# Performance work log

Measured on AMD Instinct MI355X. Metric: run time of the kernel, lower is better.

Reference implementation:

```python
import jax, jax.numpy as jnp
import numpy as np

C = 0.1          # curvature
EPS = 1e-8
BN_EPS = 1e-5
MAX_NORM = 0.9

def batchnorm_train(x, gamma, beta):
    mu = jnp.mean(x, axis=0)
    var = jnp.var(x, axis=0)  # biased, matches torch BN normalization
    return gamma * (x - mu) * jax.lax.rsqrt(var + BN_EPS) + beta

def euclidean_to_poincare(x, c=C, max_norm=MAX_NORM):
    norm = jnp.linalg.norm(x, axis=-1, keepdims=True)
    zeros_mask = norm == 0
    safe_norm = jnp.where(zeros_mask, jnp.ones_like(norm), norm)
    sqrt_c = jnp.sqrt(jnp.asarray(c, x.dtype))
    scale = max_norm * jnp.tanh(sqrt_c * norm) / (sqrt_c * safe_norm)
    return jnp.where(zeros_mask, jnp.zeros_like(x), scale * x)

def poincare_to_euclidean(x, c=C):
    norms = jnp.linalg.norm(x, axis=-1, keepdims=True)
    norms = jnp.clip(norms, 1e-8, 1.0 - 1e-8)
    sqrt_c = jnp.sqrt(jnp.asarray(c, x.dtype))
    return x * jnp.arctanh(sqrt_c * norms) / (sqrt_c * norms)

def batch_poincare_exp_map(x, v, c=C):
    x_nsq = jnp.sum(x * x, axis=-1, keepdims=True)
    lambda_x = 2.0 / (1.0 - c * x_nsq + EPS)
    v_norm = jnp.linalg.norm(v, axis=-1, keepdims=True)
    v_norm = jnp.maximum(v_norm, EPS)
    sqrt_c = jnp.sqrt(jnp.asarray(c, x.dtype))
    scale = jnp.tanh(sqrt_c * lambda_x * v_norm / 2.0) / (sqrt_c * v_norm)
    sv = scale * v
    numerator = (1.0 - c * x_nsq) * sv
    x_sv = jnp.sum(x * sv, axis=-1, keepdims=True)
    sv_nsq = jnp.sum(sv * sv, axis=-1, keepdims=True)
    denom = 1.0 - 2.0 * c * x_sv + c * c * x_nsq * sv_nsq
    result = x + numerator / (denom + EPS)
    mask = jnp.all(jnp.isfinite(result), axis=-1, keepdims=True)
    return jnp.where(mask, result, jnp.zeros_like(result))

def batch_poincare_log_map(x, y, c=C):
    x_nsq = jnp.sum(x * x, axis=-1, keepdims=True)
    lambda_x = 2.0 / (1.0 - c * x_nsq + EPS)
    y_nsq = jnp.sum(y * y, axis=-1, keepdims=True)
    xy = jnp.sum(x * y, axis=-1, keepdims=True)
    numerator = (1.0 - 2.0 * c * xy + c * y_nsq) * x - (1.0 - c * x_nsq) * y
    denom = 1.0 - 2.0 * c * xy + c * c * x_nsq * y_nsq
    diff = numerator / (denom + EPS)
    diff_norm = jnp.linalg.norm(diff, axis=-1, keepdims=True)
    diff_norm = jnp.maximum(diff_norm, EPS)
    sqrt_c = jnp.sqrt(jnp.asarray(c, x.dtype))
    return 2.0 / (sqrt_c * lambda_x) * jnp.arctanh(sqrt_c * diff_norm) * diff / diff_norm

def setup_inputs() -> dict:
    key = jax.random.key(0)
    ks = jax.random.split(key, 8)
    B, D_IN, H, D_OUT = 8192, 1024, 2048, 1000
    x = jax.random.normal(ks[0], (B, D_IN), dtype=jnp.float32)
    # kaiming_normal fan_out: std = sqrt(2/fan_out) with fan_out = out_features
    W1 = jax.random.normal(ks[1], (H, D_IN), dtype=jnp.float32) * np.sqrt(2.0 / H)
    b1 = jnp.zeros((H,), jnp.float32)
    g1 = jnp.ones((H,), jnp.float32)
    be1 = jnp.zeros((H,), jnp.float32)
    W2 = jax.random.normal(ks[2], (H, H), dtype=jnp.float32) * np.sqrt(2.0 / H)
    b2 = jnp.zeros((H,), jnp.float32)
    g2 = jnp.ones((H,), jnp.float32)
    be2 = jnp.zeros((H,), jnp.float32)
    W3 = jax.random.normal(ks[3], (D_OUT, H), dtype=jnp.float32) * np.sqrt(2.0 / D_OUT)
    b3 = jnp.zeros((D_OUT,), jnp.float32)
    return {"x": x, "W1": W1, "b1": b1, "g1": g1, "be1": be1,
            "W2": W2, "b2": b2, "g2": g2, "be2": be2, "W3": W3, "b3": b3}

def reference(x, W1, b1, g1, be1, W2, b2, g2, be2, W3, b3):
    h1 = jax.nn.relu(batchnorm_train(x @ W1.T + b1, g1, be1))
    h1_hyp = euclidean_to_poincare(h1)
    origin = jnp.zeros_like(h1_hyp)
    h1_tan = batch_poincare_log_map(origin, h1_hyp)
    h2_tan = jax.nn.relu(batchnorm_train(h1_tan @ W2.T + b2, g2, be2))
    h2_hyp = batch_poincare_exp_map(origin, h2_tan)
    h2_euc = poincare_to_euclidean(h2_hyp)
    out = h2_euc @ W3.T + b3
    return jax.nn.log_softmax(out, axis=1)
```

## Files before the change

kernel.cpp:

```cpp
#include <hip/hip_runtime.h>

typedef __bf16 bf16x8 __attribute__((ext_vector_type(8)));
typedef float f32x16 __attribute__((ext_vector_type(16)));
typedef unsigned short us8 __attribute__((ext_vector_type(8)));

#define AS1 __attribute__((address_space(1)))
#define AS3 __attribute__((address_space(3)))

__device__ __forceinline__ unsigned short f2bf(float x) {
  unsigned int u = __float_as_uint(x);
  u += 0x7fffu + ((u >> 16) & 1u);
  return (unsigned short)(u >> 16);
}
__device__ __forceinline__ float bf2f(unsigned short u) {
  return __uint_as_float(((unsigned int)u) << 16);
}
__device__ __forceinline__ void async_copy16(const void* g, void* l) {
  __builtin_amdgcn_global_load_lds((AS1 void*)(g), (AS3 void*)(l), 16, 0, 0);
}

#define BARRIER() asm volatile("s_barrier" ::: "memory")
#define WAITV(n) asm volatile("s_waitcnt vmcnt(" #n ")" ::: "memory")

__global__ void __launch_bounds__(256) k_prep(const float* __restrict__ x,
                                              const float* __restrict__ W1,
                                              const float* __restrict__ W2,
                                              const float* __restrict__ W3,
                                              unsigned short* __restrict__ Xb,
                                              unsigned short* __restrict__ W1b,
                                              unsigned short* __restrict__ W2b,
                                              unsigned short* __restrict__ W3b,
                                              float* __restrict__ P) {
  const long n1 = 2097152, n2 = 524288, n3 = 1048576, n4 = 524288;
  long i = (long)blockIdx.x * 256 + threadIdx.x;
  const float* s = nullptr;
  unsigned short* d = nullptr;
  long j = i;
  if (i < n1)                { s = x;  d = Xb; }
  else if ((j -= n1) < n2)   { s = W1; d = W1b; }
  else if ((j -= n2) < n3)   { s = W2; d = W2b; }
  else if ((j -= n3) < n4) {
    ushort4 o;
    if ((j >> 9) < 1000) {
      float4 v = ((const float4*)W3)[j];
      o.x = f2bf(v.x); o.y = f2bf(v.y); o.z = f2bf(v.z); o.w = f2bf(v.w);
    } else { o.x = 0; o.y = 0; o.z = 0; o.w = 0; }
    ((ushort4*)W3b)[j] = o;
    return;
  } else {
    j -= n4;
    ((float4*)P)[j] = (float4){0.f, 0.f, 0.f, 0.f};
    return;
  }
  float4 v = ((const float4*)s)[j];
  ushort4 o;
  o.x = f2bf(v.x); o.y = f2bf(v.y); o.z = f2bf(v.z); o.w = f2bf(v.w);
  ((ushort4*)d)[j] = o;
}

template <bool OUTBF16, bool STATS>
__global__ void __launch_bounds__(256, 1) k_gemm(const unsigned short* __restrict__ A,
                                                 const unsigned short* __restrict__ B,
                                                 void* __restrict__ Cout,
                                                 void* __restrict__ Cout2, int K,
                                                 int lda, int ldb, int ldc,
                                                 float* __restrict__ P) {
  __shared__ __align__(16) unsigned short lA[2][256 * 64];
  __shared__ __align__(16) unsigned short lB[2][256 * 64];
  const int tid = threadIdx.x;
  const int wave = tid >> 6;
  const int lane = tid & 63;
  const int l31 = lane & 31;
  const int khi = lane >> 5;
  const int r7 = l31 & 7;
  const int wrh = wave >> 1;
  const int wcn = wave & 1;

  const int f = blockIdx.x + gridDim.x * blockIdx.y;
  const int xcd = f & 7;
  const int fi = f >> 3;
  const int nblk = fi % gridDim.x;
  const int mblk = fi / gridDim.x + (gridDim.y >> 3) * xcd;
  const long m0 = (long)mblk * 256;
  const long n0 = (long)nblk * 256;
  const long koff = (long)blockIdx.z * K;
  const int NT = K >> 6;

  const int rsub = lane >> 3;
  const int qg = ((lane & 7) ^ rsub) * 8;
  const long lda8 = (long)lda * 8;
  const long ldb8 = (long)ldb * 8;
  const unsigned short* gAw = A + (m0 + wave * 64 + rsub) * (long)lda + koff + qg;
  const unsigned short* gBw = B + (n0 + wave * 64 + rsub) * (long)ldb + koff + qg;
  const int dW = (wave * 64) * 64;

  f32x16 acc[4][4];
#pragma unroll
  for (int i = 0; i < 4; ++i)
#pragma unroll
    for (int j = 0; j < 4; ++j) acc[i][j] = (f32x16)(0.f);

  auto stage = [&](int buf, long kk) {
    unsigned short* dA = &lA[buf][0] + dW;
    unsigned short* dB = &lB[buf][0] + dW;
#pragma unroll
    for (int i = 0; i < 8; ++i)
      async_copy16(gAw + (long)i * lda8 + kk, dA + i * 8 * 64);
#pragma unroll
    for (int i = 0; i < 8; ++i)
      async_copy16(gBw + (long)i * ldb8 + kk, dB + i * 8 * 64);
  };

  stage(0, 0);
  for (int t = 0; t < NT; ++t) {
    const unsigned short* lAc = &lA[t & 1][0];
    const unsigned short* lBc = &lB[t & 1][0];
    WAITV(0);
    BARRIER();
    if (t + 1 < NT) stage((t + 1) & 1, (long)(t + 1) * 64);
#pragma unroll
    for (int ks = 0; ks < 4; ++ks) {
      const int off = ((ks * 2 + khi) ^ r7) * 8;
      bf16x8 af[4], bfr[4];
#pragma unroll
      for (int m = 0; m < 4; ++m)
        af[m] = *(const bf16x8*)&lAc[(wrh * 128 + m * 32 + l31) * 64 + off];
#pragma unroll
      for (int n = 0; n < 4; ++n)
        bfr[n] = *(const bf16x8*)&lBc[(wcn * 128 + n * 32 + l31) * 64 + off];
#pragma unroll
      for (int m = 0; m < 4; ++m)
#pragma unroll
        for (int n = 0; n < 4; ++n)
          acc[m][n] = __builtin_amdgcn_mfma_f32_32x32x16_bf16(af[m], bfr[n], acc[m][n], 0, 0, 0);
    }
  }

  const int rbase = 4 * khi;
  const long crow0 = m0 + wrh * 128;
  const long ccol0 = n0 + wcn * 128;
  if (OUTBF16) {
    unsigned short* C = (unsigned short*)(blockIdx.z ? Cout2 : Cout);
#pragma unroll
    for (int m = 0; m < 4; ++m)
#pragma unroll
      for (int n = 0; n < 4; ++n) {
        long col = ccol0 + n * 32 + l31;
#pragma unroll
        for (int reg = 0; reg < 16; ++reg) {
          long row = crow0 + m * 32 + (reg & 3) + 8 * (reg >> 2) + rbase;
          C[row * (long)ldc + col] = f2bf(acc[m][n][reg]);
        }
      }
  } else {
    float* C = (float*)(blockIdx.z ? Cout2 : Cout);
#pragma unroll
    for (int m = 0; m < 4; ++m)
#pragma unroll
      for (int n = 0; n < 4; ++n) {
        long col = ccol0 + n * 32 + l31;
#pragma unroll
        for (int reg = 0; reg < 16; ++reg) {
          long row = crow0 + m * 32 + (reg & 3) + 8 * (reg >> 2) + rbase;
          C[row * (long)ldc + col] = acc[m][n][reg];
        }
      }
  }

  if (STATS) {
    float* sred = (float*)&lA[0][0];
    __syncthreads();
    sred[tid] = 0.f;
    sred[256 + tid] = 0.f;
    __syncthreads();
#pragma unroll
    for (int n = 0; n < 4; ++n) {
      float s = 0.f, s2 = 0.f;
#pragma unroll
      for (int m = 0; m < 4; ++m)
#pragma unroll
        for (int reg = 0; reg < 16; ++reg) {
          float v = acc[m][n][reg];
          s += v;
          s2 = fmaf(v, v, s2);
        }
      int cl = wcn * 128 + n * 32 + l31;
      atomicAdd(&sred[cl], s);
      atomicAdd(&sred[256 + cl], s2);
    }
    __syncthreads();
    atomicAdd(&P[n0 + tid], sred[tid]);
    atomicAdd(&P[2048 + n0 + tid], sred[256 + tid]);
  }
}

template <bool STAGE2>
__global__ void __launch_bounds__(256) k_fuse(const unsigned short* __restrict__ Zb,
                                              const float* __restrict__ P,
                                              const float* __restrict__ g,
                                              const float* __restrict__ be,
                                              unsigned short* __restrict__ Ab) {
  const int t = threadIdx.x, wave = t >> 6, lane = t & 63;
  const long row = (long)blockIdx.x * 4 + wave;

  float sc[32], sh[32];
#pragma unroll
  for (int c = 0; c < 4; ++c) {
    int b4 = (lane + 64 * c) * 2;
    float4 s0 = ((const float4*)P)[b4],       s1 = ((const float4*)P)[b4 + 1];
    float4 q0 = ((const float4*)P)[512 + b4], q1 = ((const float4*)P)[512 + b4 + 1];
    float4 g0 = ((const float4*)g)[b4],       g1 = ((const float4*)g)[b4 + 1];
    float4 e0 = ((const float4*)be)[b4],      e1 = ((const float4*)be)[b4 + 1];
    float sm[8] = {s0.x, s0.y, s0.z, s0.w, s1.x, s1.y, s1.z, s1.w};
    float sq[8] = {q0.x, q0.y, q0.z, q0.w, q1.x, q1.y, q1.z, q1.w};
    float gg[8] = {g0.x, g0.y, g0.z, g0.w, g1.x, g1.y, g1.z, g1.w};
    float bb[8] = {e0.x, e0.y, e0.z, e0.w, e1.x, e1.y, e1.z, e1.w};
#pragma unroll
    for (int j = 0; j < 8; ++j) {
      float mean = sm[j] * (1.f / 8192.f);
      float var = sq[j] * (1.f / 8192.f) - mean * mean;
      float a = gg[j] * rsqrtf(var + 1e-5f);
      sc[c * 8 + j] = a;
      sh[c * 8 + j] = bb[j] - mean * a;
    }
  }

  const us8* zr = (const us8*)(Zb + row * 2048);
  float v[32];
  float ss = 0.f;
#pragma unroll
  for (int c = 0; c < 4; ++c) {
    us8 z8 = zr[lane + 64 * c];
#pragma unroll
    for (int j = 0; j < 8; ++j) {
      float xv = fmaxf(fmaf(bf2f(z8[j]), sc[c * 8 + j], sh[c * 8 + j]), 0.f);
      v[c * 8 + j] = xv;
      ss = fmaf(xv, xv, ss);
    }
  }
#pragma unroll
  for (int o = 32; o > 0; o >>= 1) ss += __shfl_xor(ss, o, 64);
  float n2 = ss;

  const float rsc = 0.31622776601683794f;
  float fac;
  if (STAGE2) {
    float nn = sqrtf(n2);
    float vn = fmaxf(nn, 1e-8f);
    float tt = rsc * vn;
    float scl = tanhf(tt) / tt;
    float hn = scl * nn;
    float cn = fminf(fmaxf(hn, 1e-8f), 1.0f);
    float z = rsc * cn;
    fac = scl * (atanhf(z) / z);
  } else {
    fac = 0.f;
    if (n2 > 0.f) {
      float n = sqrtf(n2);
      float th = tanhf(rsc * n);
      float s = 0.9f * th / (rsc * n);
      float dn = fmaxf(s * n, 1e-8f);
      float z = rsc * dn;
      fac = -(atanhf(z) / z) * s;
    }
  }
  us8* dr = (us8*)(Ab + row * 2048);
#pragma unroll
  for (int c = 0; c < 4; ++c) {
    us8 o8;
#pragma unroll
    for (int j = 0; j < 8; ++j) o8[j] = f2bf(v[c * 8 + j] * fac);
    dr[lane + 64 * c] = o8;
  }
}

__global__ void __launch_bounds__(256) k_lsm(const unsigned short* __restrict__ Za,
                                             const unsigned short* __restrict__ Zb2,
                                             const float* __restrict__ b3,
                                             float* __restrict__ out) {
  const int t = threadIdx.x, wave = t >> 6, lane = t & 63;
  const long row = (long)blockIdx.x * 4 + wave;
  const unsigned short* za = Za + row * 1024;
  const unsigned short* zb = Zb2 + row * 1024;
  float v[16];
  float mx = -3.4e38f;
#pragma unroll
  for (int c = 0; c < 16; ++c) {
    int col = lane + 64 * c;
    if (col < 1000) {
      v[c] = bf2f(za[col]) + bf2f(zb[col]) + b3[col];
      mx = fmaxf(mx, v[c]);
    } else v[c] = -3.4e38f;
  }
#pragma unroll
  for (int o = 32; o > 0; o >>= 1) mx = fmaxf(mx, __shfl_xor(mx, o, 64));

  float se = 0.f;
#pragma unroll
  for (int c = 0; c < 16; ++c) {
    int col = lane + 64 * c;
    if (col < 1000) se += expf(v[c] - mx);
  }
#pragma unroll
  for (int o = 32; o > 0; o >>= 1) se += __shfl_xor(se, o, 64);
  float ls = logf(se);

  float* orow = out + row * 1000;
#pragma unroll
  for (int c = 0; c < 16; ++c) {
    int col = lane + 64 * c;
    if (col < 1000) orow[col] = v[c] - mx - ls;
  }
}

extern "C" void kernel_launch(void* const* d_in, const int* in_sizes, int n_in,
                              void* d_out, int out_size, void* d_ws, size_t ws_size,
                              hipStream_t stream) {
  (void)in_sizes; (void)n_in; (void)out_size; (void)ws_size;
  const float* x   = (const float*)d_in[0];
  const float* W1  = (const float*)d_in[1];
  const float* g1  = (const float*)d_in[3];
  const float* be1 = (const float*)d_in[4];
  const float* W2  = (const float*)d_in[5];
  const float* g2  = (const float*)d_in[7];
  const float* be2 = (const float*)d_in[8];
  const float* W3  = (const float*)d_in[9];
  const float* b3  = (const float*)d_in[10];
  float* out = (float*)d_out;

  char* ws = (char*)d_ws;
  size_t off = 0;
  auto alloc = [&](size_t bytes) {
    void* p = ws + off;
    off += (bytes + 255) & ~(size_t)255;
    return p;
  };
  unsigned short* Xb  = (unsigned short*)alloc((size_t)8192 * 1024 * 2);
  unsigned short* W1b = (unsigned short*)alloc((size_t)2048 * 1024 * 2);
  unsigned short* W2b = (unsigned short*)alloc((size_t)2048 * 2048 * 2);
  unsigned short* W3b = (unsigned short*)alloc((size_t)1024 * 2048 * 2);
  unsigned short* Zb  = (unsigned short*)alloc((size_t)8192 * 2048 * 2);
  unsigned short* Ab  = (unsigned short*)alloc((size_t)8192 * 2048 * 2);
  unsigned short* Z3a = (unsigned short*)alloc((size_t)8192 * 1024 * 2);
  float* P            = (float*)alloc((size_t)2 * 4096 * 4);
  float* P2 = P + 4096;
  unsigned short* Z3b = Zb;

  k_prep<<<16392, 256, 0, stream>>>(x, W1, W2, W3, Xb, W1b, W2b, W3b, P);

  k_gemm<true, true><<<dim3(8, 32, 1), 256, 0, stream>>>(Xb, W1b, Zb, Zb, 1024, 1024, 1024, 2048, P);
  k_fuse<false><<<2048, 256, 0, stream>>>(Zb, P, g1, be1, Ab);

  k_gemm<true, true><<<dim3(8, 32, 1), 256, 0, stream>>>(Ab, W2b, Zb, Zb, 2048, 2048, 2048, 2048, P2);
  k_fuse<true><<<2048, 256, 0, stream>>>(Zb, P2, g2, be2, Ab);

  k_gemm<true, false><<<dim3(4, 32, 2), 256, 0, stream>>>(Ab, W3b, Z3a, Z3b, 1024, 2048, 2048, 1024, nullptr);
  k_lsm<<<2048, 256, 0, stream>>>(Z3a, Z3b, b3, out);
}
```

Before: 336.3 us.

## Use 8 waves per GEMM block with 128x64 per-wave tiles

The GEMM block grows from 256 to 512 threads. The 256x256 tile is split across 8 waves in a 2x4 layout, so each wave computes 128x64 with half the accumulators. Global-to-LDS staging is redistributed across the 8 waves, and the column-statistics reduction is adjusted to match. This lowers register pressure and adds latency hiding per CU, at the cost of more LDS reads of the A fragments per useful MFMA and a launch bound asking for 2 blocks per CU, which the 128KB of LDS per block may not allow.

```diff
diff --git a/kernel.cpp b/kernel.cpp
--- a/kernel.cpp
+++ b/kernel.cpp
@@ -59,7 +59,7 @@
 }
 
 template <bool OUTBF16, bool STATS>
-__global__ void __launch_bounds__(256, 1) k_gemm(const unsigned short* __restrict__ A,
+__global__ void __launch_bounds__(512, 2) k_gemm(const unsigned short* __restrict__ A,
                                                  const unsigned short* __restrict__ B,
                                                  void* __restrict__ Cout,
                                                  void* __restrict__ Cout2, int K,
@@ -73,8 +73,8 @@
   const int l31 = lane & 31;
   const int khi = lane >> 5;
   const int r7 = l31 & 7;
-  const int wrh = wave >> 1;
-  const int wcn = wave & 1;
+  const int wrh = wave >> 2;
+  const int wcn = wave & 3;
 
   const int f = blockIdx.x + gridDim.x * blockIdx.y;
   const int xcd = f & 7;
@@ -88,27 +88,37 @@
 
   const int rsub = lane >> 3;
   const int qg = ((lane & 7) ^ rsub) * 8;
-  const long lda8 = (long)lda * 8;
-  const long ldb8 = (long)ldb * 8;
-  const unsigned short* gAw = A + (m0 + wave * 64 + rsub) * (long)lda + koff + qg;
-  const unsigned short* gBw = B + (n0 + wave * 64 + rsub) * (long)ldb + koff + qg;
-  const int dW = (wave * 64) * 64;
-
-  f32x16 acc[4][4];
+  const unsigned short* gAq0 = A + (m0 +       8 * wave + rsub) * (long)lda + koff + qg;
+  const unsigned short* gAq1 = A + (m0 +  64 + 8 * wave + rsub) * (long)lda + koff + qg;
+  const unsigned short* gAq2 = A + (m0 + 128 + 8 * wave + rsub) * (long)lda + koff + qg;
+  const unsigned short* gAq3 = A + (m0 + 192 + 8 * wave + rsub) * (long)lda + koff + qg;
+  const unsigned short* gB0  = B + (n0 + 32 * wave + rsub) * (long)ldb + koff + qg;
+  const unsigned short* gB1  = gB0 +  8 * (long)ldb;
+  const unsigned short* gB2  = gB0 + 16 * (long)ldb;
+  const unsigned short* gB3  = gB0 + 24 * (long)ldb;
+  const int dAq0 = (      8 * wave) * 64;
+  const int dAq1 = ( 64 + 8 * wave) * 64;
+  const int dAq2 = (128 + 8 * wave) * 64;
+  const int dAq3 = (192 + 8 * wave) * 64;
+  const int dB0  = (32 * wave) * 64;
+
+  f32x16 acc[4][2];
 #pragma unroll
   for (int i = 0; i < 4; ++i)
 #pragma unroll
-    for (int j = 0; j < 4; ++j) acc[i][j] = (f32x16)(0.f);
+    for (int j = 0; j < 2; ++j) acc[i][j] = (f32x16)(0.f);
 
   auto stage = [&](int buf, long kk) {
-    unsigned short* dA = &lA[buf][0] + dW;
-    unsigned short* dB = &lB[buf][0] + dW;
-#pragma unroll
-    for (int i = 0; i < 8; ++i)
-      async_copy16(gAw + (long)i * lda8 + kk, dA + i * 8 * 64);
-#pragma unroll
-    for (int i = 0; i < 8; ++i)
-      async_copy16(gBw + (long)i * ldb8 + kk, dB + i * 8 * 64);
+    unsigned short* lAn = &lA[buf][0];
+    unsigned short* lBn = &lB[buf][0];
+    async_copy16(gAq0 + kk, lAn + dAq0);
+    async_copy16(gAq1 + kk, lAn + dAq1);
+    async_copy16(gAq2 + kk, lAn + dAq2);
+    async_copy16(gAq3 + kk, lAn + dAq3);
+    async_copy16(gB0 + kk,  lBn + dB0);
+    async_copy16(gB1 + kk,  lBn + dB0 + 8 * 64);
+    async_copy16(gB2 + kk,  lBn + dB0 + 16 * 64);
+    async_copy16(gB3 + kk,  lBn + dB0 + 24 * 64);
   };
 
   stage(0, 0);
@@ -121,30 +131,30 @@
 #pragma unroll
     for (int ks = 0; ks < 4; ++ks) {
       const int off = ((ks * 2 + khi) ^ r7) * 8;
-      bf16x8 af[4], bfr[4];
+      bf16x8 af[4], bfr[2];
 #pragma unroll
       for (int m = 0; m < 4; ++m)
         af[m] = *(const bf16x8*)&lAc[(wrh * 128 + m * 32 + l31) * 64 + off];
 #pragma unroll
-      for (int n = 0; n < 4; ++n)
-        bfr[n] = *(const bf16x8*)&lBc[(wcn * 128 + n * 32 + l31) * 64 + off];
+      for (int n = 0; n < 2; ++n)
+        bfr[n] = *(const bf16x8*)&lBc[(wcn * 64 + n * 32 + l31) * 64 + off];
 #pragma unroll
       for (int m = 0; m < 4; ++m)
 #pragma unroll
-        for (int n = 0; n < 4; ++n)
+        for (int n = 0; n < 2; ++n)
           acc[m][n] = __builtin_amdgcn_mfma_f32_32x32x16_bf16(af[m], bfr[n], acc[m][n], 0, 0, 0);
     }
   }
 
   const int rbase = 4 * khi;
   const long crow0 = m0 + wrh * 128;
-  const long ccol0 = n0 + wcn * 128;
+  const long ccol0 = n0 + wcn * 64;
   if (OUTBF16) {
     unsigned short* C = (unsigned short*)(blockIdx.z ? Cout2 : Cout);
 #pragma unroll
     for (int m = 0; m < 4; ++m)
 #pragma unroll
-      for (int n = 0; n < 4; ++n) {
+      for (int n = 0; n < 2; ++n) {
         long col = ccol0 + n * 32 + l31;
 #pragma unroll
         for (int reg = 0; reg < 16; ++reg) {
@@ -157,7 +167,7 @@
 #pragma unroll
     for (int m = 0; m < 4; ++m)
 #pragma unroll
-      for (int n = 0; n < 4; ++n) {
+      for (int n = 0; n < 2; ++n) {
         long col = ccol0 + n * 32 + l31;
 #pragma unroll
         for (int reg = 0; reg < 16; ++reg) {
@@ -171,10 +181,9 @@
     float* sred = (float*)&lA[0][0];
     __syncthreads();
     sred[tid] = 0.f;
-    sred[256 + tid] = 0.f;
     __syncthreads();
 #pragma unroll
-    for (int n = 0; n < 4; ++n) {
+    for (int n = 0; n < 2; ++n) {
       float s = 0.f, s2 = 0.f;
 #pragma unroll
       for (int m = 0; m < 4; ++m)
@@ -184,13 +193,13 @@
           s += v;
           s2 = fmaf(v, v, s2);
         }
-      int cl = wcn * 128 + n * 32 + l31;
+      int cl = wcn * 64 + n * 32 + l31;
       atomicAdd(&sred[cl], s);
       atomicAdd(&sred[256 + cl], s2);
     }
     __syncthreads();
-    atomicAdd(&P[n0 + tid], sred[tid]);
-    atomicAdd(&P[2048 + n0 + tid], sred[256 + tid]);
+    if (tid < 256) atomicAdd(&P[n0 + tid], sred[tid]);
+    else           atomicAdd(&P[2048 + n0 + tid - 256], sred[tid]);
   }
 }
 
@@ -348,12 +357,12 @@
 
   k_prep<<<16392, 256, 0, stream>>>(x, W1, W2, W3, Xb, W1b, W2b, W3b, P);
 
-  k_gemm<true, true><<<dim3(8, 32, 1), 256, 0, stream>>>(Xb, W1b, Zb, Zb, 1024, 1024, 1024, 2048, P);
+  k_gemm<true, true><<<dim3(8, 32, 1), 512, 0, stream>>>(Xb, W1b, Zb, Zb, 1024, 1024, 1024, 2048, P);
   k_fuse<false><<<2048, 256, 0, stream>>>(Zb, P, g1, be1, Ab);
 
-  k_gemm<true, true><<<dim3(8, 32, 1), 256, 0, stream>>>(Ab, W2b, Zb, Zb, 2048, 2048, 2048, 2048, P2);
+  k_gemm<true, true><<<dim3(8, 32, 1), 512, 0, stream>>>(Ab, W2b, Zb, Zb, 2048, 2048, 2048, 2048, P2);
   k_fuse<true><<<2048, 256, 0, stream>>>(Zb, P2, g2, be2, Ab);
 
-  k_gemm<true, false><<<dim3(4, 32, 2), 256, 0, stream>>>(Ab, W3b, Z3a, Z3b, 1024, 2048, 2048, 1024, nullptr);
+  k_gemm<true, false><<<dim3(4, 32, 2), 512, 0, stream>>>(Ab, W3b, Z3a, Z3b, 1024, 2048, 2048, 1024, nullptr);
   k_lsm<<<2048, 256, 0, stream>>>(Z3a, Z3b, b3, out);
 }
```

After: 317.6 us. 5.6% less time.
